# Kernel optimization log

Measured on AMD Instinct MI355X. Metric: run time of the kernel, lower is better.

Reference implementation:

```python
import jax, jax.numpy as jnp
import numpy as np

N = 4096        # num gaussians
H = 128         # image height
W = 128         # image width
ZOOM = 0.5
EPS = 1e-6


def _normalize(q):
    # torch F.normalize(dim=1): q / max(||q||, 1e-12)
    n = jnp.linalg.norm(q, axis=1, keepdims=True)
    return q / jnp.maximum(n, 1e-12)


def _left_quat_matrix(q):
    # q: (N,4) = (w,x,y,z); left-multiplication matrix L(q) so that q*p = L(q) p
    w, x, y, z = q[:, 0], q[:, 1], q[:, 2], q[:, 3]
    return jnp.stack([
        jnp.stack([w, -x, -y, -z], -1),
        jnp.stack([x,  w, -z,  y], -1),
        jnp.stack([y,  z,  w, -x], -1),
        jnp.stack([z, -y,  x,  w], -1)], axis=1)


def _right_quat_matrix_conj(q):
    # right-multiplication matrix of conj(q): R(conj(q)) = R(q)^T
    w, x, y, z = q[:, 0], q[:, 1], q[:, 2], q[:, 3]
    return jnp.stack([
        jnp.stack([ w,  x,  y,  z], -1),
        jnp.stack([-x,  w,  z, -y], -1),
        jnp.stack([-y, -z,  w,  x], -1),
        jnp.stack([-z,  y, -x,  w], -1)], axis=1)


def setup_inputs() -> dict:
    key = jax.random.key(0)
    k1, k2, k3, k4, k5 = jax.random.split(key, 5)
    means = jax.random.normal(k1, (N, 4), dtype=jnp.float32)
    raw_scales = jax.random.normal(k2, (N, 4), dtype=jnp.float32)
    rotors = jax.random.normal(k3, (N, 8), dtype=jnp.float32)
    t = jax.random.uniform(k4, (), dtype=jnp.float32)
    angle = jax.random.uniform(k5, (), dtype=jnp.float32)
    return {"means": means, "raw_scales": raw_scales, "rotors": rotors,
            "t": t, "angle": angle}


def reference(means, raw_scales, rotors, t, angle):
    scale = jnp.exp(raw_scales)                              # (N,4)
    sign = jnp.array([1.0, -1.0, -1.0, -1.0], jnp.float32)
    q1 = _normalize(rotors[:, jnp.array([0, 4, 5, 6])])
    q2 = _normalize(rotors[:, jnp.array([7, 1, 2, 3])] * sign)
    L = _left_quat_matrix(q1)                                # (N,4,4)
    Rm = _right_quat_matrix_conj(q2)                         # (N,4,4)
    R4 = jnp.einsum('nij,njk->nik', L, Rm)                   # (N,4,4)
    # cov4D = R4 diag(scale^2) R4^T
    cov4D = jnp.einsum('nij,nj,nkj->nik', R4, scale * scale, R4)

    U = cov4D[:, :3, :3]                                     # (N,3,3)
    V = cov4D[:, :3, 3]                                      # (N,3)
    Wm = jnp.maximum(cov4D[:, 3, 3], EPS)                    # (N,)
    lambda_t = 1.0 / Wm

    mu_xyz = means[:, :3]
    mu_t = means[:, 3]
    time_diff = t - mu_t                                     # (N,)
    mu3D = mu_xyz + V * (time_diff / Wm)[:, None]            # (N,3)

    sin_a, cos_a = jnp.sin(angle), jnp.cos(angle)
    z0, o1 = jnp.zeros(()), jnp.ones(())
    view = jnp.stack([jnp.stack([cos_a, z0, sin_a]),
                      jnp.stack([z0, o1, z0]),
                      jnp.stack([-sin_a, z0, cos_a])])       # (3,3)

    mu3D_view = mu3D @ view.T                                # (N,3)
    cov3D = U - jnp.einsum('ni,nj->nij', V, V) / Wm[:, None, None]
    cov3D_view = jnp.einsum('ij,njk,lk->nil', view, cov3D, view)

    scale_mat = jnp.array([[(W - 1) / 2 * ZOOM, 0.0, 0.0],
                           [0.0, (H - 1) / 2 * ZOOM, 0.0]], jnp.float32)
    offset = jnp.array([(W - 1) / 2, (H - 1) / 2], jnp.float32)
    mu2D = mu3D_view @ scale_mat.T + offset                  # (N,2)
    cov2D = jnp.einsum('ij,njk,lk->nil', scale_mat, cov3D_view, scale_mat)
    cov2D = cov2D + jnp.eye(2, dtype=jnp.float32) * EPS      # (N,2,2)

    # analytic 2x2 inverse (same as torch.linalg.inv for 2x2)
    a, b = cov2D[:, 0, 0], cov2D[:, 0, 1]
    c, d = cov2D[:, 1, 0], cov2D[:, 1, 1]
    det = a * d - b * c
    inv_cov2D = jnp.stack([jnp.stack([d, -b], -1),
                           jnp.stack([-c, a], -1)], axis=1) / det[:, None, None]

    weights = jnp.exp(-0.5 * lambda_t * time_diff ** 2)      # (N,)

    yy, xx = jnp.meshgrid(jnp.arange(H, dtype=jnp.float32),
                          jnp.arange(W, dtype=jnp.float32), indexing='ij')
    grid = jnp.stack([xx, yy], -1).reshape(-1, 2)            # (P,2), P=H*W

    delta = grid[None, :, :] - mu2D[:, None, :]              # (N,P,2)
    expo = -0.5 * jnp.einsum('npi,nij,npj->np', delta, inv_cov2D, delta)
    patch = weights[:, None] * jnp.exp(expo)                 # (N,P)
    image = patch.sum(axis=0).reshape(H, W)
    image = image / jnp.maximum(image.max(), EPS)
    return image
```

## Files before the change

### kernel.cpp

```cpp
#include <hip/hip_runtime.h>
#include <math.h>

#define NG   4096
#define HH   128
#define WW   128
#define NPIX (HH*WW)
#define EPSF 1e-6f
#define CHUNK 128
#define NCH  (NG/CHUNK)
#define PXT  4
#define PXB  (NPIX/(256*PXT))

#if __has_builtin(__builtin_amdgcn_exp2f)
#define EXP2F(x) __builtin_amdgcn_exp2f(x)
#else
#define EXP2F(x) exp2f(x)
#endif

__global__ __launch_bounds__(256) void prep_kernel(
    const float* __restrict__ means, const float* __restrict__ raw_scales,
    const float* __restrict__ rotors, const float* __restrict__ tp,
    const float* __restrict__ ap, float* __restrict__ params,
    float* __restrict__ acc)
{
    int i = blockIdx.x * 256 + threadIdx.x;
    if (i >= NG) return;

    ((float4*)acc)[i] = make_float4(0.f, 0.f, 0.f, 0.f);

    float t = tp[0], angle = ap[0];

    float r0 = rotors[i*8+0], r1 = rotors[i*8+1], r2 = rotors[i*8+2], r3 = rotors[i*8+3];
    float r4 = rotors[i*8+4], r5 = rotors[i*8+5], r6 = rotors[i*8+6], r7 = rotors[i*8+7];

    float w1 = r0, x1 = r4, y1 = r5, z1 = r6;
    float n1 = fmaxf(sqrtf(w1*w1 + x1*x1 + y1*y1 + z1*z1), 1e-12f);
    w1 /= n1; x1 /= n1; y1 /= n1; z1 /= n1;
    float w2 = r7, x2 = -r1, y2 = -r2, z2 = -r3;
    float n2 = fmaxf(sqrtf(w2*w2 + x2*x2 + y2*y2 + z2*z2), 1e-12f);
    w2 /= n2; x2 /= n2; y2 /= n2; z2 /= n2;

    float L[4][4]  = {{w1,-x1,-y1,-z1},{x1,w1,-z1,y1},{y1,z1,w1,-x1},{z1,-y1,x1,w1}};
    float Rm[4][4] = {{w2, x2, y2, z2},{-x2,w2,z2,-y2},{-y2,-z2,w2,x2},{-z2,y2,-x2,w2}};

    float R4[4][4];
    #pragma unroll
    for (int a = 0; a < 4; ++a)
        #pragma unroll
        for (int b = 0; b < 4; ++b)
            R4[a][b] = L[a][0]*Rm[0][b] + L[a][1]*Rm[1][b] + L[a][2]*Rm[2][b] + L[a][3]*Rm[3][b];

    float s2[4];
    #pragma unroll
    for (int j = 0; j < 4; ++j) {
        float e = expf(raw_scales[i*4+j]);
        s2[j] = e * e;
    }

    float cov[4][4];
    #pragma unroll
    for (int a = 0; a < 4; ++a)
        #pragma unroll
        for (int b = a; b < 4; ++b) {
            float s = R4[a][0]*s2[0]*R4[b][0] + R4[a][1]*s2[1]*R4[b][1]
                    + R4[a][2]*s2[2]*R4[b][2] + R4[a][3]*s2[3]*R4[b][3];
            cov[a][b] = s; cov[b][a] = s;
        }

    float Wm   = fmaxf(cov[3][3], EPSF);
    float invW = 1.0f / Wm;
    float V0 = cov[0][3], V1 = cov[1][3], V2 = cov[2][3];
    float td = t - means[i*4+3];

    float mu0 = means[i*4+0] + V0 * td * invW;
    float mu1 = means[i*4+1] + V1 * td * invW;
    float mu2 = means[i*4+2] + V2 * td * invW;

    float ca = cosf(angle), sa = sinf(angle);
    float mvx = ca*mu0 + sa*mu2;
    float mvy = mu1;

    float C00 = cov[0][0] - V0*V0*invW;
    float C01 = cov[0][1] - V0*V1*invW;
    float C02 = cov[0][2] - V0*V2*invW;
    float C11 = cov[1][1] - V1*V1*invW;
    float C12 = cov[1][2] - V1*V2*invW;
    float C22 = cov[2][2] - V2*V2*invW;

    float cv00 = ca*ca*C00 + 2.f*ca*sa*C02 + sa*sa*C22;
    float cv01 = ca*C01 + sa*C12;
    float cv11 = C11;

    const float Ksc = 31.75f;
    const float K2  = Ksc * Ksc;
    float a = K2*cv00 + EPSF;
    float b = K2*cv01;
    float d = K2*cv11 + EPSF;
    float det = a*d - b*b;
    float invdet = 1.0f / det;

    const float L2E = 1.4426950408889634f;
    float A  = -0.5f * d * invdet * L2E;
    float B  =         b * invdet * L2E;
    float C  = -0.5f * a * invdet * L2E;
    float c0 = -0.5f * invW * td * td * L2E;

    float mux = Ksc*mvx + 63.5f;
    float muy = Ksc*mvy + 63.5f;

    float* p = params + i*8;
    p[0] = mux; p[1] = muy; p[2] = A; p[3] = B;
    p[4] = C;   p[5] = c0;  p[6] = A + A; p[7] = 0.f;
}

__global__ __launch_bounds__(256) void accum_kernel(
    const float* __restrict__ params, float* __restrict__ acc)
{
    __shared__ float sp[CHUNK*8];
    int tid = threadIdx.x;
    int pxb = blockIdx.x & (PXB-1);
    int ch  = blockIdx.x / PXB;

    ((float4*)sp)[tid] = ((const float4*)(params + ch*CHUNK*8))[tid];
    __syncthreads();

    float px = (float)((tid & 31) * PXT);
    float py = (float)(pxb * 8 + (tid >> 5));

    float a0 = 0.f, a1 = 0.f, a2 = 0.f, a3 = 0.f;
    #pragma unroll 4
    for (int g = 0; g < CHUNK; ++g) {
        const float* q = sp + g*8;
        float4 v0 = *(const float4*)(q);
        float4 v1 = *(const float4*)(q + 4);
        float dx = px - v0.x;
        float dy = py - v0.y;
        float b1 = v0.w * dy;
        float tt = fmaf(v1.x * dy, dy, v1.y);
        float e  = fmaf(fmaf(v0.z, dx, b1), dx, tt);
        float dd = fmaf(v0.z, fmaf(2.f, dx, 1.f), b1);
        a0 += EXP2F(e); e += dd; dd += v1.z;
        a1 += EXP2F(e); e += dd; dd += v1.z;
        a2 += EXP2F(e); e += dd;
        a3 += EXP2F(e);
    }

    float* ap = acc + pxb*1024 + (tid >> 5)*128 + (tid & 31)*PXT;
    atomicAdd(ap+0, a0); atomicAdd(ap+1, a1);
    atomicAdd(ap+2, a2); atomicAdd(ap+3, a3);
}

__global__ __launch_bounds__(256) void norm_kernel(
    const float* __restrict__ acc, float* __restrict__ out)
{
    int tid = threadIdx.x;
    float m = 0.f;
    #pragma unroll 8
    for (int i = 0; i < NPIX/256; ++i)
        m = fmaxf(m, acc[i*256 + tid]);
    #pragma unroll
    for (int off = 32; off > 0; off >>= 1)
        m = fmaxf(m, __shfl_xor(m, off));
    __shared__ float sm[4];
    if ((tid & 63) == 0) sm[tid >> 6] = m;
    __syncthreads();
    m = fmaxf(fmaxf(sm[0], sm[1]), fmaxf(sm[2], sm[3]));
    m = fmaxf(m, EPSF);
    float inv = 1.0f / m;
    int p = blockIdx.x*256 + tid;
    out[p] = acc[p] * inv;
}

extern "C" void kernel_launch(void* const* d_in, const int* in_sizes, int n_in,
                              void* d_out, int out_size, void* d_ws, size_t ws_size,
                              hipStream_t stream) {
    const float* means      = (const float*)d_in[0];
    const float* raw_scales = (const float*)d_in[1];
    const float* rotors     = (const float*)d_in[2];
    const float* t          = (const float*)d_in[3];
    const float* angle      = (const float*)d_in[4];
    float* out = (float*)d_out;

    float* params = (float*)d_ws;
    float* acc    = params + NG*8;

    prep_kernel<<<NG/256, 256, 0, stream>>>(means, raw_scales, rotors, t, angle, params, acc);
    accum_kernel<<<PXB*NCH, 256, 0, stream>>>(params, acc);
    norm_kernel<<<NPIX/256, 256, 0, stream>>>(acc, out);
}
```

Measured before the change: 92.80 us.

## Replace atomic accumulation with per-chunk partials and a deterministic reduction pass

```diff
diff --git a/kernel.cpp b/kernel.cpp
--- a/kernel.cpp
+++ b/kernel.cpp
@@ -6,7 +6,7 @@
 #define WW   128
 #define NPIX (HH*WW)
 #define EPSF 1e-6f
-#define CHUNK 128
+#define CHUNK 64
 #define NCH  (NG/CHUNK)
 #define PXT  4
 #define PXB  (NPIX/(256*PXT))
@@ -20,14 +20,10 @@
 __global__ __launch_bounds__(256) void prep_kernel(
     const float* __restrict__ means, const float* __restrict__ raw_scales,
     const float* __restrict__ rotors, const float* __restrict__ tp,
-    const float* __restrict__ ap, float* __restrict__ params,
-    float* __restrict__ acc)
+    const float* __restrict__ ap, float* __restrict__ params)
 {
     int i = blockIdx.x * 256 + threadIdx.x;
     if (i >= NG) return;
-
-    ((float4*)acc)[i] = make_float4(0.f, 0.f, 0.f, 0.f);
-
     float t = tp[0], angle = ap[0];
 
     float r0 = rotors[i*8+0], r1 = rotors[i*8+1], r2 = rotors[i*8+2], r3 = rotors[i*8+3];
@@ -113,15 +109,16 @@
     p[4] = C;   p[5] = c0;  p[6] = A + A; p[7] = 0.f;
 }
 
-__global__ __launch_bounds__(256) void accum_kernel(
-    const float* __restrict__ params, float* __restrict__ acc)
+__global__ __launch_bounds__(256) void raster_kernel(
+    const float* __restrict__ params, float* __restrict__ partials)
 {
     __shared__ float sp[CHUNK*8];
     int tid = threadIdx.x;
     int pxb = blockIdx.x & (PXB-1);
     int ch  = blockIdx.x / PXB;
 
-    ((float4*)sp)[tid] = ((const float4*)(params + ch*CHUNK*8))[tid];
+    if (tid < CHUNK*2)
+        ((float4*)sp)[tid] = ((const float4*)(params + ch*CHUNK*8))[tid];
     __syncthreads();
 
     float px = (float)((tid & 31) * PXT);
@@ -145,26 +142,41 @@
         a3 += EXP2F(e);
     }
 
-    float* ap = acc + pxb*1024 + (tid >> 5)*128 + (tid & 31)*PXT;
-    atomicAdd(ap+0, a0); atomicAdd(ap+1, a1);
-    atomicAdd(ap+2, a2); atomicAdd(ap+3, a3);
-}
-
-__global__ __launch_bounds__(256) void norm_kernel(
-    const float* __restrict__ acc, float* __restrict__ out)
+    ((float4*)(partials + ch*NPIX + pxb*1024))[tid] = make_float4(a0, a1, a2, a3);
+}
+
+__global__ __launch_bounds__(256) void reduce_kernel(
+    const float* __restrict__ partials, float* __restrict__ acc,
+    float* __restrict__ bmax)
 {
     int tid = threadIdx.x;
-    float m = 0.f;
+    int p = blockIdx.x*256 + tid;
+    float s = 0.f;
     #pragma unroll 8
-    for (int i = 0; i < NPIX/256; ++i)
-        m = fmaxf(m, acc[i*256 + tid]);
+    for (int ch = 0; ch < NCH; ++ch)
+        s += partials[ch*NPIX + p];
+    acc[p] = s;
+
+    float m = s;
     #pragma unroll
     for (int off = 32; off > 0; off >>= 1)
         m = fmaxf(m, __shfl_xor(m, off));
     __shared__ float sm[4];
     if ((tid & 63) == 0) sm[tid >> 6] = m;
     __syncthreads();
-    m = fmaxf(fmaxf(sm[0], sm[1]), fmaxf(sm[2], sm[3]));
+    if (tid == 0)
+        bmax[blockIdx.x] = fmaxf(fmaxf(sm[0], sm[1]), fmaxf(sm[2], sm[3]));
+}
+
+__global__ __launch_bounds__(256) void norm_kernel(
+    const float* __restrict__ acc, const float* __restrict__ bmax,
+    float* __restrict__ out)
+{
+    int tid = threadIdx.x;
+    float m = bmax[tid & 63];
+    #pragma unroll
+    for (int off = 32; off > 0; off >>= 1)
+        m = fmaxf(m, __shfl_xor(m, off));
     m = fmaxf(m, EPSF);
     float inv = 1.0f / m;
     int p = blockIdx.x*256 + tid;
@@ -181,10 +193,13 @@
     const float* angle      = (const float*)d_in[4];
     float* out = (float*)d_out;
 
-    float* params = (float*)d_ws;
-    float* acc    = params + NG*8;
-
-    prep_kernel<<<NG/256, 256, 0, stream>>>(means, raw_scales, rotors, t, angle, params, acc);
-    accum_kernel<<<PXB*NCH, 256, 0, stream>>>(params, acc);
-    norm_kernel<<<NPIX/256, 256, 0, stream>>>(acc, out);
-}
+    float* params   = (float*)d_ws;
+    float* partials = params + NG*8;
+    float* acc      = partials + NCH*NPIX;
+    float* bmax     = acc + NPIX;
+
+    prep_kernel<<<NG/256, 256, 0, stream>>>(means, raw_scales, rotors, t, angle, params);
+    raster_kernel<<<PXB*NCH, 256, 0, stream>>>(params, partials);
+    reduce_kernel<<<NPIX/256, 256, 0, stream>>>(partials, acc, bmax);
+    norm_kernel<<<NPIX/256, 256, 0, stream>>>(acc, bmax, out);
+}
```

After: 83.80 us. -9.7%, faster.
